# Kernel tuning notes

Measured on AMD Instinct MI355X. Metric: run time of the kernel, lower is better.

Reference implementation:

```python
import jax, jax.numpy as jnp
import numpy as np

B, S, HID = 1, 2048, 2048
H, HK, D, DV = 16, 4, 128, 128
ROPE = 64  # head_dim * partial_rotary_factor
SCALE = D ** -0.5


def _rotate_half(x):
    x1, x2 = x[..., : x.shape[-1] // 2], x[..., x.shape[-1] // 2:]
    return jnp.concatenate((-x2, x1), axis=-1)


def setup_inputs() -> dict:
    key = jax.random.key(0)
    ks = jax.random.split(key, 6)
    hidden_states = jax.random.normal(ks[0], (B, S, HID), dtype=jnp.float32)
    # real RoPE tables: positions x inv_freq over rope_dim, HF half-duplicated layout
    inv_freq = 1.0 / (10000.0 ** (jnp.arange(0, ROPE, 2, dtype=jnp.float32) / ROPE))
    ang = jnp.arange(S, dtype=jnp.float32)[:, None] * inv_freq[None, :]  # [S, ROPE/2]
    ang = jnp.concatenate([ang, ang], axis=-1)  # [S, ROPE]
    cos = jnp.broadcast_to(jnp.cos(ang)[None], (B, S, ROPE))
    sin = jnp.broadcast_to(jnp.sin(ang)[None], (B, S, ROPE))
    Wq = jax.random.normal(ks[1], (HID, H * D), dtype=jnp.float32) * 0.02
    Wk = jax.random.normal(ks[2], (HID, HK * D), dtype=jnp.float32) * 0.02
    Wv = jax.random.normal(ks[3], (HID, HK * DV), dtype=jnp.float32) * 0.02
    Wo = jax.random.normal(ks[4], (H * DV, HID), dtype=jnp.float32) * 0.02
    sink = jax.random.normal(ks[5], (H,), dtype=jnp.float32)
    return {"hidden_states": hidden_states, "cos": cos, "sin": sin,
            "Wq": Wq, "Wk": Wk, "Wv": Wv, "Wo": Wo, "sink": sink}


def reference(hidden_states, cos, sin, Wq, Wk, Wv, Wo, sink):
    b, s, _ = hidden_states.shape
    q = (hidden_states @ Wq).reshape(b, s, H, D).transpose(0, 2, 1, 3)    # [B,H,S,D]
    k = (hidden_states @ Wk).reshape(b, s, HK, D).transpose(0, 2, 1, 3)   # [B,HK,S,D]
    v = (hidden_states @ Wv).reshape(b, s, HK, DV).transpose(0, 2, 1, 3)  # [B,HK,S,DV]
    # partial RoPE on the first ROPE dims
    c = cos[:, None, :, :]  # [B,1,S,ROPE]
    sn = sin[:, None, :, :]
    q_r, q_n = q[..., :ROPE], q[..., ROPE:]
    k_r, k_n = k[..., :ROPE], k[..., ROPE:]
    q_r = q_r * c + _rotate_half(q_r) * sn
    k_r = k_r * c + _rotate_half(k_r) * sn
    q = jnp.concatenate([q_r, q_n], axis=-1)
    k = jnp.concatenate([k_r, k_n], axis=-1)
    # GQA: repeat kv heads
    g = H // HK
    k = jnp.broadcast_to(k[:, :, None], (b, HK, g, s, D)).reshape(b, H, s, D)
    v = jnp.broadcast_to(v[:, :, None], (b, HK, g, s, DV)).reshape(b, H, s, DV)
    scores = jnp.einsum("bhqd,bhkd->bhqk", q, k) * SCALE
    causal = jnp.triu(jnp.ones((s, s), dtype=bool), k=1)
    scores = jnp.where(causal[None, None], -jnp.inf, scores)
    # sink-bias softmax: sink logit joins the normalizer but gets no value
    m = jnp.max(scores, axis=-1, keepdims=True)                      # [B,H,S,1]
    sink_exp = jnp.exp(sink.reshape(1, H, 1, 1) - m)
    attn_exp = jnp.exp(scores - m)
    attn = attn_exp / (jnp.sum(attn_exp, axis=-1, keepdims=True) + sink_exp)
    out = jnp.einsum("bhqk,bhkv->bhqv", attn, v)                     # [B,H,S,DV]
    out = out.transpose(0, 2, 1, 3).reshape(b, s, H * DV)
    return out @ Wo
```

## Files before the change

### kernel.cpp

```cpp
#include <hip/hip_runtime.h>

#define S_LEN 2048
#define HID_D 2048
#define NH 16
#define NHK 4
#define HD 128
#define ATT_SCALE 0.08838834764831845f
#define NEG_INF (-3.0e38f)

typedef __attribute__((ext_vector_type(8))) __bf16 bf16x8;
typedef __attribute__((ext_vector_type(4))) __bf16 bf16x4;
typedef __attribute__((ext_vector_type(4))) float f32x4;

__device__ __forceinline__ void gload_lds16(const void* g, void* l) {
  __builtin_amdgcn_global_load_lds(
      (__attribute__((address_space(1))) void*)g,
      (__attribute__((address_space(3))) void*)l, 16, 0, 0);
}

__device__ __forceinline__ void transpose_job(
    const float* __restrict__ W, __bf16* __restrict__ WT, int K, int N,
    int local, int nbx, float* Ts ) {
  const int t = threadIdx.x;
  const int bk = (local / nbx) * 64, bn = (local % nbx) * 64;
  const int r = t >> 4, c4 = (t & 15) << 2;
#pragma unroll
  for (int i = 0; i < 4; ++i) {
    float4 v = *reinterpret_cast<const float4*>(
        &W[(size_t)(bk + r + 16 * i) * N + bn + c4]);
    *reinterpret_cast<float4*>(&Ts[(r + 16 * i) * 68 + c4]) = v;
  }
  __syncthreads();
#pragma unroll
  for (int i = 0; i < 4; ++i) {
    int n_l = r + 16 * i;
    bf16x4 o;
#pragma unroll
    for (int j = 0; j < 4; ++j) o[j] = (__bf16)Ts[(c4 + j) * 68 + n_l];
    *reinterpret_cast<bf16x4*>(&WT[(size_t)(bn + n_l) * K + bk + c4]) = o;
  }
}

__global__ __launch_bounds__(256) void prep_kernel(
    const float* __restrict__ hs, const float* __restrict__ Wq,
    const float* __restrict__ Wk, const float* __restrict__ Wv,
    const float* __restrict__ Wo, __bf16* __restrict__ hsb,
    __bf16* __restrict__ WqT, __bf16* __restrict__ WkT,
    __bf16* __restrict__ WvT, __bf16* __restrict__ WoT) {
  __shared__ float Ts[64 * 68];
  const int b = blockIdx.x;
  if (b < 4096) {
    int i = b * 256 + threadIdx.x;
    if (i < S_LEN * HID_D / 4) {
      float4 v = *reinterpret_cast<const float4*>(&hs[(size_t)i * 4]);
      bf16x4 o;
      o[0] = (__bf16)v.x; o[1] = (__bf16)v.y;
      o[2] = (__bf16)v.z; o[3] = (__bf16)v.w;
      *reinterpret_cast<bf16x4*>(&hsb[(size_t)i * 4]) = o;
    }
  } else if (b < 5120) {
    transpose_job(Wq, WqT, 2048, 2048, b - 4096, 32, Ts);
  } else if (b < 5376) {
    transpose_job(Wk, WkT, 2048, 512, b - 5120, 8, Ts);
  } else if (b < 5632) {
    transpose_job(Wv, WvT, 2048, 512, b - 5376, 8, Ts);
  } else {
    transpose_job(Wo, WoT, 2048, 2048, b - 5632, 32, Ts);
  }
}

template <int MODE>
__device__ __forceinline__ void mfma_gemm_tile_db(
    __bf16* As, __bf16* Bs,
    const __bf16* __restrict__ A, const __bf16* __restrict__ BT,
    float* __restrict__ C, __bf16* __restrict__ Db,
    const float* __restrict__ cs, const float* __restrict__ sn,
    int N, int K, int bm, int bn) {
  const int tid = threadIdx.x;
  const int wave = tid >> 6, lane = tid & 63;
  const int wr = (wave >> 1) * 64, wc = (wave & 1) * 64;
  const int l16 = lane & 15, lhi = lane >> 4;

  f32x4 acc[4][4];
#pragma unroll
  for (int i = 0; i < 4; ++i)
#pragma unroll
    for (int j = 0; j < 4; ++j) acc[i][j] = (f32x4){0.f, 0.f, 0.f, 0.f};

  const __bf16* Abase = A + (size_t)bm * K;
  const __bf16* Bbase = BT + (size_t)bn * K;
  const int nk = K >> 6;

  auto stage = [&](int buf, int k0) {
#pragma unroll
    for (int it = 0; it < 4; ++it) {
      int base = it * 256 + wave * 64;
      int f = base + lane;
      int row = f >> 3, ch = f & 7;
      gload_lds16(Abase + (size_t)row * K + k0 + ch * 8,
                  As + buf * 8192 + base * 8);
      gload_lds16(Bbase + (size_t)row * K + k0 + ch * 8,
                  Bs + buf * 8192 + base * 8);
    }
  };

  stage(0, 0);
  __syncthreads();
  for (int t = 0; t < nk; ++t) {
    const int buf = t & 1;
    if (t + 1 < nk) stage(buf ^ 1, (t + 1) * 64);
    const __bf16* Ab = As + buf * 8192;
    const __bf16* Bb = Bs + buf * 8192;
#pragma unroll
    for (int kk = 0; kk < 2; ++kk) {
      bf16x8 af[4], bfr[4];
#pragma unroll
      for (int i = 0; i < 4; ++i) {
        af[i] = *reinterpret_cast<const bf16x8*>(
            Ab + (wr + i * 16 + l16) * 64 + kk * 32 + lhi * 8);
        bfr[i] = *reinterpret_cast<const bf16x8*>(
            Bb + (wc + i * 16 + l16) * 64 + kk * 32 + lhi * 8);
      }
#pragma unroll
      for (int i = 0; i < 4; ++i)
#pragma unroll
        for (int j = 0; j < 4; ++j)
          acc[i][j] = __builtin_amdgcn_mfma_f32_16x16x32_bf16(
              af[i], bfr[j], acc[i][j], 0, 0, 0);
    }
    __syncthreads();
  }

  if (MODE == 0) {
#pragma unroll
    for (int i = 0; i < 4; ++i)
#pragma unroll
      for (int j = 0; j < 4; ++j)
#pragma unroll
        for (int r = 0; r < 4; ++r)
          C[(size_t)(bm + wr + i * 16 + lhi * 4 + r) * N + bn + wc + j * 16 +
            l16] = acc[i][j][r];
  } else if (MODE == 3) {
#pragma unroll
    for (int i = 0; i < 4; ++i)
#pragma unroll
      for (int j = 0; j < 4; ++j) {
        bf16x4 o;
#pragma unroll
        for (int r = 0; r < 4; ++r) o[r] = (__bf16)acc[i][j][r];
        *reinterpret_cast<bf16x4*>(
            &Db[(size_t)(bn + wc + j * 16 + l16) * S_LEN + bm + wr + i * 16 +
                lhi * 4]) = o;
      }
  } else {
    const int dst = (MODE == 1) ? (NH * HD) : (NHK * HD);
    if (wc == 0) {
#pragma unroll
      for (int i = 0; i < 4; ++i)
#pragma unroll
        for (int r = 0; r < 4; ++r) {
          int s = bm + wr + i * 16 + lhi * 4 + r;
          const float* cp = cs + (size_t)s * 64;
          const float* sp = sn + (size_t)s * 64;
          float c0 = cp[l16], c1 = cp[16 + l16];
          float c2 = cp[32 + l16], c3 = cp[48 + l16];
          float s0 = sp[l16], s1 = sp[16 + l16];
          float s2 = sp[32 + l16], s3 = sp[48 + l16];
          float x0 = acc[i][0][r], x1 = acc[i][1][r];
          float x2 = acc[i][2][r], x3 = acc[i][3][r];
          __bf16* dp = Db + (size_t)s * dst + bn;
          dp[l16]      = (__bf16)(x0 * c0 - x2 * s0);
          dp[16 + l16] = (__bf16)(x1 * c1 - x3 * s1);
          dp[32 + l16] = (__bf16)(x2 * c2 + x0 * s2);
          dp[48 + l16] = (__bf16)(x3 * c3 + x1 * s3);
        }
    } else {
#pragma unroll
      for (int i = 0; i < 4; ++i)
#pragma unroll
        for (int j = 0; j < 4; ++j)
#pragma unroll
          for (int r = 0; r < 4; ++r)
            Db[(size_t)(bm + wr + i * 16 + lhi * 4 + r) * dst + bn + wc +
               j * 16 + l16] = (__bf16)acc[i][j][r];
    }
  }
}

__global__ __launch_bounds__(256, 2) void qkv_gemm_kernel(
    const __bf16* __restrict__ hsb, const __bf16* __restrict__ WqT,
    const __bf16* __restrict__ WkT, const __bf16* __restrict__ WvT,
    __bf16* __restrict__ Qbf, __bf16* __restrict__ Kbf,
    __bf16* __restrict__ Vtb, const float* __restrict__ cs,
    const float* __restrict__ sn) {
  __shared__ __attribute__((aligned(16))) __bf16 As[2 * 8192];
  __shared__ __attribute__((aligned(16))) __bf16 Bs[2 * 8192];
  const int bx = blockIdx.x;
  const int bm = blockIdx.y * 128;
  if (bx < 16)
    mfma_gemm_tile_db<1>(As, Bs, hsb, WqT, nullptr, Qbf, cs, sn, 2048, HID_D,
                         bm, bx * 128);
  else if (bx < 20)
    mfma_gemm_tile_db<2>(As, Bs, hsb, WkT, nullptr, Kbf, cs, sn, 512, HID_D,
                         bm, (bx - 16) * 128);
  else
    mfma_gemm_tile_db<3>(As, Bs, hsb, WvT, nullptr, Vtb, cs, sn, 512, HID_D,
                         bm, (bx - 20) * 128);
}

__global__ __launch_bounds__(256, 2) void out_proj_kernel(
    const __bf16* __restrict__ Obf, const __bf16* __restrict__ WoT,
    float* __restrict__ out) {
  __shared__ __attribute__((aligned(16))) __bf16 As[2 * 8192];
  __shared__ __attribute__((aligned(16))) __bf16 Bs[2 * 8192];
  mfma_gemm_tile_db<0>(As, Bs, Obf, WoT, out, nullptr, nullptr, nullptr,
                       HID_D, NH * HD, blockIdx.y * 128, blockIdx.x * 128);
}

__device__ __forceinline__ unsigned pack2_bf16(float a, float b) {
  unsigned short lo = __builtin_bit_cast(unsigned short, (__bf16)a);
  unsigned short hi = __builtin_bit_cast(unsigned short, (__bf16)b);
  return (unsigned)lo | ((unsigned)hi << 16);
}

__global__ __launch_bounds__(256, 2) void attn_mfma_kernel(
    const __bf16* __restrict__ Qbf, const __bf16* __restrict__ Kbf,
    const __bf16* __restrict__ Vtb, const float* __restrict__ sink,
    __bf16* __restrict__ Obf) {
  __shared__ __attribute__((aligned(16))) __bf16 Ks[2 * 64 * 128];
  __shared__ __attribute__((aligned(16))) __bf16 Vs[2 * 128 * 64];

  const int tid = threadIdx.x;
  const int wave = tid >> 6, lane = tid & 63;
  const int l16 = lane & 15, lhi = lane >> 4;
  const int h = blockIdx.y;
  const int hk = h >> 2;
  const int qt = (h < 8) ? (31 - (int)blockIdx.x) : (int)blockIdx.x;
  const int q0 = qt * 64;
  const int qrow = q0 + wave * 16 + l16;

  bf16x8 qf[4];
  {
    const __bf16* qp = Qbf + (size_t)qrow * (NH * HD) + h * HD + lhi * 8;
#pragma unroll
    for (int d = 0; d < 4; ++d)
      qf[d] = *reinterpret_cast<const bf16x8*>(qp + d * 32);
  }

  float m = NEG_INF, l_ = 0.f;
  f32x4 acc[8];
#pragma unroll
  for (int f = 0; f < 8; ++f) acc[f] = (f32x4){0.f, 0.f, 0.f, 0.f};

  auto stage_kv = [&](int buf, int kt) {
#pragma unroll
    for (int it = 0; it < 4; ++it) {
      int base = it * 256 + wave * 64;
      int f = base + lane;
      {
        int row = f >> 4, ch = f & 15;
        int sch = (ch & 8) | ((ch ^ row) & 7);
        gload_lds16(Kbf + (size_t)(kt * 64 + row) * (NHK * HD) + hk * HD +
                        sch * 8,
                    Ks + buf * 8192 + base * 8);
      }
      {
        int dv = f >> 3, ch = f & 7;
        int sch = (ch ^ dv) & 7;
        gload_lds16(Vtb + (size_t)(hk * HD + dv) * S_LEN + kt * 64 + sch * 8,
                    Vs + buf * 8192 + base * 8);
      }
    }
  };

  const int xs7 = l16 & 7;
  const int nt = qt + 1;
  stage_kv(0, 0);
  __syncthreads();
  for (int kt = 0; kt < nt; ++kt) {
    const int buf = kt & 1;
    if (kt + 1 < nt) stage_kv(buf ^ 1, kt + 1);
    const __bf16* Kb_ = Ks + buf * 8192;
    const __bf16* Vb_ = Vs + buf * 8192;

    f32x4 sc[4];
#pragma unroll
    for (int kb = 0; kb < 4; ++kb) sc[kb] = (f32x4){0.f, 0.f, 0.f, 0.f};
#pragma unroll
    for (int d = 0; d < 4; ++d) {
#pragma unroll
      for (int kb = 0; kb < 4; ++kb) {
        int row = kb * 16 + l16;
        int ch = (d * 4 + lhi) ^ xs7;
        bf16x8 kf = *reinterpret_cast<const bf16x8*>(Kb_ + row * 128 + ch * 8);
        sc[kb] = __builtin_amdgcn_mfma_f32_16x16x32_bf16(kf, qf[d], sc[kb],
                                                         0, 0, 0);
      }
    }

    float s[4][4];
    const bool last = (kt == qt);
#pragma unroll
    for (int kb = 0; kb < 4; ++kb)
#pragma unroll
      for (int r = 0; r < 4; ++r) {
        float sv = sc[kb][r] * ATT_SCALE;
        if (last) {
          int kc = kt * 64 + kb * 16 + lhi * 4 + r;
          if (kc > qrow) sv = NEG_INF;
        }
        s[kb][r] = sv;
      }
    float tmax = s[0][0];
#pragma unroll
    for (int kb = 0; kb < 4; ++kb)
#pragma unroll
      for (int r = 0; r < 4; ++r) tmax = fmaxf(tmax, s[kb][r]);
    tmax = fmaxf(tmax, __shfl_xor(tmax, 16));
    tmax = fmaxf(tmax, __shfl_xor(tmax, 32));
    float mn = fmaxf(m, tmax);
    float fac = __expf(m - mn);
    m = mn;
    float p[4][4];
    float rs = 0.f;
#pragma unroll
    for (int kb = 0; kb < 4; ++kb)
#pragma unroll
      for (int r = 0; r < 4; ++r) {
        float pv = __expf(s[kb][r] - mn);
        p[kb][r] = pv;
        rs += pv;
      }
    rs += __shfl_xor(rs, 16);
    rs += __shfl_xor(rs, 32);
    l_ = l_ * fac + rs;

    float facb[4];
#pragma unroll
    for (int r = 0; r < 4; ++r) facb[r] = __shfl(fac, lhi * 4 + r);
#pragma unroll
    for (int f = 0; f < 8; ++f)
#pragma unroll
      for (int r = 0; r < 4; ++r) acc[f][r] *= facb[r];

    unsigned pk[4][2];
#pragma unroll
    for (int kb = 0; kb < 4; ++kb) {
      pk[kb][0] = pack2_bf16(p[kb][0], p[kb][1]);
      pk[kb][1] = pack2_bf16(p[kb][2], p[kb][3]);
    }
    const int s0 = l16 + 16 * (2 * (lhi & 1));
    const int s1 = s0 + 16;
    const bool hihalf = (lhi >= 2);
    bf16x8 pa[2];
#pragma unroll
    for (int c = 0; c < 2; ++c) {
      unsigned aw0 = __shfl((int)pk[2 * c][0], s0);
      unsigned aw1 = __shfl((int)pk[2 * c][1], s0);
      unsigned aw2 = __shfl((int)pk[2 * c][0], s1);
      unsigned aw3 = __shfl((int)pk[2 * c][1], s1);
      unsigned bw0 = __shfl((int)pk[2 * c + 1][0], s0);
      unsigned bw1 = __shfl((int)pk[2 * c + 1][1], s0);
      unsigned bw2 = __shfl((int)pk[2 * c + 1][0], s1);
      unsigned bw3 = __shfl((int)pk[2 * c + 1][1], s1);
      uint4 w;
      w.x = hihalf ? bw0 : aw0;
      w.y = hihalf ? bw1 : aw1;
      w.z = hihalf ? bw2 : aw2;
      w.w = hihalf ? bw3 : aw3;
      pa[c] = __builtin_bit_cast(bf16x8, w);
    }

#pragma unroll
    for (int c = 0; c < 2; ++c) {
#pragma unroll
      for (int dvf = 0; dvf < 8; ++dvf) {
        int row = dvf * 16 + l16;
        int ch = (c * 4 + lhi) ^ xs7;
        bf16x8 vf = *reinterpret_cast<const bf16x8*>(Vb_ + row * 64 + ch * 8);
        acc[dvf] = __builtin_amdgcn_mfma_f32_16x16x32_bf16(pa[c], vf, acc[dvf],
                                                           0, 0, 0);
      }
    }
    if (kt + 1 < nt) __syncthreads();
  }

  float inv = 1.0f / (l_ + __expf(sink[h] - m));
  float invb[4];
#pragma unroll
  for (int r = 0; r < 4; ++r) invb[r] = __shfl(inv, lhi * 4 + r);
#pragma unroll
  for (int dvf = 0; dvf < 8; ++dvf)
#pragma unroll
    for (int r = 0; r < 4; ++r) {
      int row = q0 + wave * 16 + lhi * 4 + r;
      Obf[(size_t)row * (NH * HD) + h * HD + dvf * 16 + l16] =
          (__bf16)(acc[dvf][r] * invb[r]);
    }
}

extern "C" void kernel_launch(void* const* d_in, const int* in_sizes, int n_in,
                              void* d_out, int out_size, void* d_ws,
                              size_t ws_size, hipStream_t stream) {
  const float* hs   = (const float*)d_in[0];
  const float* cosb = (const float*)d_in[1];
  const float* sinb = (const float*)d_in[2];
  const float* Wq   = (const float*)d_in[3];
  const float* Wk   = (const float*)d_in[4];
  const float* Wv   = (const float*)d_in[5];
  const float* Wo   = (const float*)d_in[6];
  const float* sink = (const float*)d_in[7];
  float* out = (float*)d_out;

  __bf16* hsb = (__bf16*)d_ws;
  __bf16* WqT = hsb + (size_t)S_LEN * HID_D;
  __bf16* WkT = WqT + (size_t)HID_D * (NH * HD);
  __bf16* WvT = WkT + (size_t)HID_D * (NHK * HD);
  __bf16* WoT = WvT + (size_t)HID_D * (NHK * HD);
  __bf16* Qbf = WoT + (size_t)(NH * HD) * HID_D;
  __bf16* Kbf = Qbf + (size_t)S_LEN * (NH * HD);
  __bf16* Vtb = Kbf + (size_t)S_LEN * (NHK * HD);
  __bf16* Obf = WqT;

  prep_kernel<<<dim3(6656), 256, 0, stream>>>(hs, Wq, Wk, Wv, Wo, hsb, WqT,
                                              WkT, WvT, WoT);
  qkv_gemm_kernel<<<dim3(24, 16), 256, 0, stream>>>(hsb, WqT, WkT, WvT, Qbf,
                                                    Kbf, Vtb, cosb, sinb);
  attn_mfma_kernel<<<dim3(32, 16), 256, 0, stream>>>(Qbf, Kbf, Vtb, sink, Obf);
  out_proj_kernel<<<dim3(16, 16), 256, 0, stream>>>(Obf, WoT, out);
}
```

Before: 274.8 us.

## Swizzle GEMM LDS layout, split-K out-projection, lazy softmax rescale

The GEMM LDS tiles are XOR-swizzled by row to cut bank conflicts on the fragment reads. The output projection becomes split-K over two z-slices that accumulate with float atomics into a buffer zeroed by a memset, which doubles the block count from 256 tiles. The attention online softmax now rescales the accumulator and running sum only when some row's max grows by more than 8, skipping the per-tile exp and rescale. The trade-offs are atomic traffic plus an extra memset, and a bounded risk of larger exponent values in the unnormalized accumulators.

```diff
diff --git a/kernel.cpp b/kernel.cpp
--- a/kernel.cpp
+++ b/kernel.cpp
@@ -75,11 +75,12 @@
     const __bf16* __restrict__ A, const __bf16* __restrict__ BT,
     float* __restrict__ C, __bf16* __restrict__ Db,
     const float* __restrict__ cs, const float* __restrict__ sn,
-    int N, int K, int bm, int bn) {
+    int N, int K, int bm, int bn, int kbeg, int ksteps) {
   const int tid = threadIdx.x;
   const int wave = tid >> 6, lane = tid & 63;
   const int wr = (wave >> 1) * 64, wc = (wave & 1) * 64;
   const int l16 = lane & 15, lhi = lane >> 4;
+  const int xs7 = l16 & 7;
 
   f32x4 acc[4][4];
 #pragma unroll
@@ -89,7 +90,6 @@
 
   const __bf16* Abase = A + (size_t)bm * K;
   const __bf16* Bbase = BT + (size_t)bn * K;
-  const int nk = K >> 6;
 
   auto stage = [&](int buf, int k0) {
 #pragma unroll
@@ -97,18 +97,19 @@
       int base = it * 256 + wave * 64;
       int f = base + lane;
       int row = f >> 3, ch = f & 7;
-      gload_lds16(Abase + (size_t)row * K + k0 + ch * 8,
+      int sch = (ch ^ row) & 7;
+      gload_lds16(Abase + (size_t)row * K + k0 + sch * 8,
                   As + buf * 8192 + base * 8);
-      gload_lds16(Bbase + (size_t)row * K + k0 + ch * 8,
+      gload_lds16(Bbase + (size_t)row * K + k0 + sch * 8,
                   Bs + buf * 8192 + base * 8);
     }
   };
 
-  stage(0, 0);
+  stage(0, kbeg);
   __syncthreads();
-  for (int t = 0; t < nk; ++t) {
+  for (int t = 0; t < ksteps; ++t) {
     const int buf = t & 1;
-    if (t + 1 < nk) stage(buf ^ 1, (t + 1) * 64);
+    if (t + 1 < ksteps) stage(buf ^ 1, kbeg + (t + 1) * 64);
     const __bf16* Ab = As + buf * 8192;
     const __bf16* Bb = Bs + buf * 8192;
 #pragma unroll
@@ -116,10 +117,11 @@
       bf16x8 af[4], bfr[4];
 #pragma unroll
       for (int i = 0; i < 4; ++i) {
+        int ch = (kk * 4 + lhi) ^ xs7;
         af[i] = *reinterpret_cast<const bf16x8*>(
-            Ab + (wr + i * 16 + l16) * 64 + kk * 32 + lhi * 8);
+            Ab + (wr + i * 16 + l16) * 64 + ch * 8);
         bfr[i] = *reinterpret_cast<const bf16x8*>(
-            Bb + (wc + i * 16 + l16) * 64 + kk * 32 + lhi * 8);
+            Bb + (wc + i * 16 + l16) * 64 + ch * 8);
       }
 #pragma unroll
       for (int i = 0; i < 4; ++i)
@@ -140,6 +142,16 @@
         for (int r = 0; r < 4; ++r)
           C[(size_t)(bm + wr + i * 16 + lhi * 4 + r) * N + bn + wc + j * 16 +
             l16] = acc[i][j][r];
+  } else if (MODE == 4) {
+#pragma unroll
+    for (int i = 0; i < 4; ++i)
+#pragma unroll
+      for (int j = 0; j < 4; ++j)
+#pragma unroll
+        for (int r = 0; r < 4; ++r)
+          atomicAdd(&C[(size_t)(bm + wr + i * 16 + lhi * 4 + r) * N + bn + wc +
+                       j * 16 + l16],
+                    acc[i][j][r]);
   } else if (MODE == 3) {
 #pragma unroll
     for (int i = 0; i < 4; ++i)
@@ -199,13 +211,13 @@
   const int bm = blockIdx.y * 128;
   if (bx < 16)
     mfma_gemm_tile_db<1>(As, Bs, hsb, WqT, nullptr, Qbf, cs, sn, 2048, HID_D,
-                         bm, bx * 128);
+                         bm, bx * 128, 0, 32);
   else if (bx < 20)
     mfma_gemm_tile_db<2>(As, Bs, hsb, WkT, nullptr, Kbf, cs, sn, 512, HID_D,
-                         bm, (bx - 16) * 128);
+                         bm, (bx - 16) * 128, 0, 32);
   else
     mfma_gemm_tile_db<3>(As, Bs, hsb, WvT, nullptr, Vtb, cs, sn, 512, HID_D,
-                         bm, (bx - 20) * 128);
+                         bm, (bx - 20) * 128, 0, 32);
 }
 
 __global__ __launch_bounds__(256, 2) void out_proj_kernel(
@@ -213,8 +225,9 @@
     float* __restrict__ out) {
   __shared__ __attribute__((aligned(16))) __bf16 As[2 * 8192];
   __shared__ __attribute__((aligned(16))) __bf16 Bs[2 * 8192];
-  mfma_gemm_tile_db<0>(As, Bs, Obf, WoT, out, nullptr, nullptr, nullptr,
-                       HID_D, NH * HD, blockIdx.y * 128, blockIdx.x * 128);
+  mfma_gemm_tile_db<4>(As, Bs, Obf, WoT, out, nullptr, nullptr, nullptr,
+                       HID_D, NH * HD, blockIdx.y * 128, blockIdx.x * 128,
+                       blockIdx.z * 1024, 16);
 }
 
 __device__ __forceinline__ unsigned pack2_bf16(float a, float b) {
@@ -318,30 +331,34 @@
       for (int r = 0; r < 4; ++r) tmax = fmaxf(tmax, s[kb][r]);
     tmax = fmaxf(tmax, __shfl_xor(tmax, 16));
     tmax = fmaxf(tmax, __shfl_xor(tmax, 32));
-    float mn = fmaxf(m, tmax);
-    float fac = __expf(m - mn);
-    m = mn;
+
+    if (!__all(tmax - m <= 8.0f)) {
+      float mn = fmaxf(m, tmax);
+      float fac = __expf(m - mn);
+      l_ *= fac;
+      float facb[4];
+#pragma unroll
+      for (int r = 0; r < 4; ++r) facb[r] = __shfl(fac, lhi * 4 + r);
+#pragma unroll
+      for (int f = 0; f < 8; ++f)
+#pragma unroll
+        for (int r = 0; r < 4; ++r) acc[f][r] *= facb[r];
+      m = mn;
+    }
+
     float p[4][4];
     float rs = 0.f;
 #pragma unroll
     for (int kb = 0; kb < 4; ++kb)
 #pragma unroll
       for (int r = 0; r < 4; ++r) {
-        float pv = __expf(s[kb][r] - mn);
+        float pv = __expf(s[kb][r] - m);
         p[kb][r] = pv;
         rs += pv;
       }
     rs += __shfl_xor(rs, 16);
     rs += __shfl_xor(rs, 32);
-    l_ = l_ * fac + rs;
-
-    float facb[4];
-#pragma unroll
-    for (int r = 0; r < 4; ++r) facb[r] = __shfl(fac, lhi * 4 + r);
-#pragma unroll
-    for (int f = 0; f < 8; ++f)
-#pragma unroll
-      for (int r = 0; r < 4; ++r) acc[f][r] *= facb[r];
+    l_ += rs;
 
     unsigned pk[4][2];
 #pragma unroll
@@ -427,5 +444,6 @@
   qkv_gemm_kernel<<<dim3(24, 16), 256, 0, stream>>>(hsb, WqT, WkT, WvT, Qbf,
                                                     Kbf, Vtb, cosb, sinb);
   attn_mfma_kernel<<<dim3(32, 16), 256, 0, stream>>>(Qbf, Kbf, Vtb, sink, Obf);
-  out_proj_kernel<<<dim3(16, 16), 256, 0, stream>>>(Obf, WoT, out);
-}
+  hipMemsetAsync(out, 0, (size_t)S_LEN * HID_D * sizeof(float), stream);
+  out_proj_kernel<<<dim3(16, 16, 2), 256, 0, stream>>>(Obf, WoT, out);
+}
```

Result: faster. 259.6 us (-5.5%).

## Shrink GEMM M-tile, swizzle LDS, single-buffer attention with lazy rescale and exp2

Applied to the files above, without the earlier changes.

The GEMM tiles drop from 128x128 to 64x128 so the grids double, and an XOR swizzle is added to the LDS layout to cut bank conflicts. The attention kernel moves from double-buffered to single-buffered K/V staging, which halves LDS use but exposes load latency on every tile. It also switches to exp2 with a prescaled log2e and skips the rescale of the accumulator unless the running max grows past a threshold. Priority hints are placed around the MFMA blocks. Together these are meant to raise occupancy and cut per-tile exponent and rescale work.

```diff
diff --git a/kernel.cpp b/kernel.cpp
--- a/kernel.cpp
+++ b/kernel.cpp
@@ -6,11 +6,15 @@
 #define NHK 4
 #define HD 128
 #define ATT_SCALE 0.08838834764831845f
+#define LOG2E 1.4426950408889634f
+#define SCALE2 (ATT_SCALE * LOG2E)
 #define NEG_INF (-3.0e38f)
 
 typedef __attribute__((ext_vector_type(8))) __bf16 bf16x8;
 typedef __attribute__((ext_vector_type(4))) __bf16 bf16x4;
 typedef __attribute__((ext_vector_type(4))) float f32x4;
+
+#define EXP2F(x) __builtin_amdgcn_exp2f(x)
 
 __device__ __forceinline__ void gload_lds16(const void* g, void* l) {
   __builtin_amdgcn_global_load_lds(
@@ -78,12 +82,13 @@
     int N, int K, int bm, int bn) {
   const int tid = threadIdx.x;
   const int wave = tid >> 6, lane = tid & 63;
-  const int wr = (wave >> 1) * 64, wc = (wave & 1) * 64;
+  const int wr = (wave >> 1) * 32, wc = (wave & 1) * 64;
   const int l16 = lane & 15, lhi = lane >> 4;
-
-  f32x4 acc[4][4];
-#pragma unroll
-  for (int i = 0; i < 4; ++i)
+  const int xs7 = l16 & 7;
+
+  f32x4 acc[2][4];
+#pragma unroll
+  for (int i = 0; i < 2; ++i)
 #pragma unroll
     for (int j = 0; j < 4; ++j) acc[i][j] = (f32x4){0.f, 0.f, 0.f, 0.f};
 
@@ -93,14 +98,21 @@
 
   auto stage = [&](int buf, int k0) {
 #pragma unroll
-    for (int it = 0; it < 4; ++it) {
+    for (int it = 0; it < 6; ++it) {
       int base = it * 256 + wave * 64;
       int f = base + lane;
-      int row = f >> 3, ch = f & 7;
-      gload_lds16(Abase + (size_t)row * K + k0 + ch * 8,
-                  As + buf * 8192 + base * 8);
-      gload_lds16(Bbase + (size_t)row * K + k0 + ch * 8,
-                  Bs + buf * 8192 + base * 8);
+      if (base < 512) {
+        int row = f >> 3, ch = f & 7;
+        int sch = (ch ^ row) & 7;
+        gload_lds16(Abase + (size_t)row * K + k0 + sch * 8,
+                    As + buf * 4096 + base * 8);
+      } else {
+        int g = f - 512;
+        int row = g >> 3, ch = g & 7;
+        int sch = (ch ^ row) & 7;
+        gload_lds16(Bbase + (size_t)row * K + k0 + sch * 8,
+                    Bs + buf * 8192 + (base - 512) * 8);
+      }
     }
   };
 
@@ -109,20 +121,22 @@
   for (int t = 0; t < nk; ++t) {
     const int buf = t & 1;
     if (t + 1 < nk) stage(buf ^ 1, (t + 1) * 64);
-    const __bf16* Ab = As + buf * 8192;
+    const __bf16* Ab = As + buf * 4096;
     const __bf16* Bb = Bs + buf * 8192;
 #pragma unroll
     for (int kk = 0; kk < 2; ++kk) {
-      bf16x8 af[4], bfr[4];
-#pragma unroll
-      for (int i = 0; i < 4; ++i) {
+      int ch = (kk * 4 + lhi) ^ xs7;
+      bf16x8 af[2], bfr[4];
+#pragma unroll
+      for (int i = 0; i < 2; ++i)
         af[i] = *reinterpret_cast<const bf16x8*>(
-            Ab + (wr + i * 16 + l16) * 64 + kk * 32 + lhi * 8);
-        bfr[i] = *reinterpret_cast<const bf16x8*>(
-            Bb + (wc + i * 16 + l16) * 64 + kk * 32 + lhi * 8);
-      }
-#pragma unroll
-      for (int i = 0; i < 4; ++i)
+            Ab + (wr + i * 16 + l16) * 64 + ch * 8);
+#pragma unroll
+      for (int j = 0; j < 4; ++j)
+        bfr[j] = *reinterpret_cast<const bf16x8*>(
+            Bb + (wc + j * 16 + l16) * 64 + ch * 8);
+#pragma unroll
+      for (int i = 0; i < 2; ++i)
 #pragma unroll
         for (int j = 0; j < 4; ++j)
           acc[i][j] = __builtin_amdgcn_mfma_f32_16x16x32_bf16(
@@ -133,7 +147,7 @@
 
   if (MODE == 0) {
 #pragma unroll
-    for (int i = 0; i < 4; ++i)
+    for (int i = 0; i < 2; ++i)
 #pragma unroll
       for (int j = 0; j < 4; ++j)
 #pragma unroll
@@ -142,7 +156,7 @@
             l16] = acc[i][j][r];
   } else if (MODE == 3) {
 #pragma unroll
-    for (int i = 0; i < 4; ++i)
+    for (int i = 0; i < 2; ++i)
 #pragma unroll
       for (int j = 0; j < 4; ++j) {
         bf16x4 o;
@@ -156,7 +170,7 @@
     const int dst = (MODE == 1) ? (NH * HD) : (NHK * HD);
     if (wc == 0) {
 #pragma unroll
-      for (int i = 0; i < 4; ++i)
+      for (int i = 0; i < 2; ++i)
 #pragma unroll
         for (int r = 0; r < 4; ++r) {
           int s = bm + wr + i * 16 + lhi * 4 + r;
@@ -176,7 +190,7 @@
         }
     } else {
 #pragma unroll
-      for (int i = 0; i < 4; ++i)
+      for (int i = 0; i < 2; ++i)
 #pragma unroll
         for (int j = 0; j < 4; ++j)
 #pragma unroll
@@ -193,10 +207,10 @@
     __bf16* __restrict__ Qbf, __bf16* __restrict__ Kbf,
     __bf16* __restrict__ Vtb, const float* __restrict__ cs,
     const float* __restrict__ sn) {
-  __shared__ __attribute__((aligned(16))) __bf16 As[2 * 8192];
+  __shared__ __attribute__((aligned(16))) __bf16 As[2 * 4096];
   __shared__ __attribute__((aligned(16))) __bf16 Bs[2 * 8192];
   const int bx = blockIdx.x;
-  const int bm = blockIdx.y * 128;
+  const int bm = blockIdx.y * 64;
   if (bx < 16)
     mfma_gemm_tile_db<1>(As, Bs, hsb, WqT, nullptr, Qbf, cs, sn, 2048, HID_D,
                          bm, bx * 128);
@@ -211,10 +225,10 @@
 __global__ __launch_bounds__(256, 2) void out_proj_kernel(
     const __bf16* __restrict__ Obf, const __bf16* __restrict__ WoT,
     float* __restrict__ out) {
-  __shared__ __attribute__((aligned(16))) __bf16 As[2 * 8192];
+  __shared__ __attribute__((aligned(16))) __bf16 As[2 * 4096];
   __shared__ __attribute__((aligned(16))) __bf16 Bs[2 * 8192];
   mfma_gemm_tile_db<0>(As, Bs, Obf, WoT, out, nullptr, nullptr, nullptr,
-                       HID_D, NH * HD, blockIdx.y * 128, blockIdx.x * 128);
+                       HID_D, NH * HD, blockIdx.y * 64, blockIdx.x * 128);
 }
 
 __device__ __forceinline__ unsigned pack2_bf16(float a, float b) {
@@ -227,8 +241,8 @@
     const __bf16* __restrict__ Qbf, const __bf16* __restrict__ Kbf,
     const __bf16* __restrict__ Vtb, const float* __restrict__ sink,
     __bf16* __restrict__ Obf) {
-  __shared__ __attribute__((aligned(16))) __bf16 Ks[2 * 64 * 128];
-  __shared__ __attribute__((aligned(16))) __bf16 Vs[2 * 128 * 64];
+  __shared__ __attribute__((aligned(16))) __bf16 Ks[64 * 128];
+  __shared__ __attribute__((aligned(16))) __bf16 Vs[128 * 64];
 
   const int tid = threadIdx.x;
   const int wave = tid >> 6, lane = tid & 63;
@@ -252,7 +266,9 @@
 #pragma unroll
   for (int f = 0; f < 8; ++f) acc[f] = (f32x4){0.f, 0.f, 0.f, 0.f};
 
-  auto stage_kv = [&](int buf, int kt) {
+  const int xs7 = l16 & 7;
+  const int nt = qt + 1;
+  for (int kt = 0; kt < nt; ++kt) {
 #pragma unroll
     for (int it = 0; it < 4; ++it) {
       int base = it * 256 + wave * 64;
@@ -262,41 +278,33 @@
         int sch = (ch & 8) | ((ch ^ row) & 7);
         gload_lds16(Kbf + (size_t)(kt * 64 + row) * (NHK * HD) + hk * HD +
                         sch * 8,
-                    Ks + buf * 8192 + base * 8);
+                    Ks + base * 8);
       }
       {
         int dv = f >> 3, ch = f & 7;
         int sch = (ch ^ dv) & 7;
         gload_lds16(Vtb + (size_t)(hk * HD + dv) * S_LEN + kt * 64 + sch * 8,
-                    Vs + buf * 8192 + base * 8);
-      }
-    }
-  };
-
-  const int xs7 = l16 & 7;
-  const int nt = qt + 1;
-  stage_kv(0, 0);
-  __syncthreads();
-  for (int kt = 0; kt < nt; ++kt) {
-    const int buf = kt & 1;
-    if (kt + 1 < nt) stage_kv(buf ^ 1, kt + 1);
-    const __bf16* Kb_ = Ks + buf * 8192;
-    const __bf16* Vb_ = Vs + buf * 8192;
+                    Vs + base * 8);
+      }
+    }
+    __syncthreads();
 
     f32x4 sc[4];
 #pragma unroll
     for (int kb = 0; kb < 4; ++kb) sc[kb] = (f32x4){0.f, 0.f, 0.f, 0.f};
+    __builtin_amdgcn_s_setprio(1);
 #pragma unroll
     for (int d = 0; d < 4; ++d) {
 #pragma unroll
       for (int kb = 0; kb < 4; ++kb) {
         int row = kb * 16 + l16;
         int ch = (d * 4 + lhi) ^ xs7;
-        bf16x8 kf = *reinterpret_cast<const bf16x8*>(Kb_ + row * 128 + ch * 8);
+        bf16x8 kf = *reinterpret_cast<const bf16x8*>(Ks + row * 128 + ch * 8);
         sc[kb] = __builtin_amdgcn_mfma_f32_16x16x32_bf16(kf, qf[d], sc[kb],
                                                          0, 0, 0);
       }
     }
+    __builtin_amdgcn_s_setprio(0);
 
     float s[4][4];
     const bool last = (kt == qt);
@@ -304,7 +312,7 @@
     for (int kb = 0; kb < 4; ++kb)
 #pragma unroll
       for (int r = 0; r < 4; ++r) {
-        float sv = sc[kb][r] * ATT_SCALE;
+        float sv = sc[kb][r] * SCALE2;
         if (last) {
           int kc = kt * 64 + kb * 16 + lhi * 4 + r;
           if (kc > qrow) sv = NEG_INF;
@@ -318,30 +326,34 @@
       for (int r = 0; r < 4; ++r) tmax = fmaxf(tmax, s[kb][r]);
     tmax = fmaxf(tmax, __shfl_xor(tmax, 16));
     tmax = fmaxf(tmax, __shfl_xor(tmax, 32));
-    float mn = fmaxf(m, tmax);
-    float fac = __expf(m - mn);
-    m = mn;
+
+    if (!__all(tmax - m <= 11.54f)) {
+      float mn = fmaxf(m, tmax);
+      float fac = EXP2F(m - mn);
+      l_ *= fac;
+      float facb[4];
+#pragma unroll
+      for (int r = 0; r < 4; ++r) facb[r] = __shfl(fac, lhi * 4 + r);
+#pragma unroll
+      for (int f = 0; f < 8; ++f)
+#pragma unroll
+        for (int r = 0; r < 4; ++r) acc[f][r] *= facb[r];
+      m = mn;
+    }
+
     float p[4][4];
     float rs = 0.f;
 #pragma unroll
     for (int kb = 0; kb < 4; ++kb)
 #pragma unroll
       for (int r = 0; r < 4; ++r) {
-        float pv = __expf(s[kb][r] - mn);
+        float pv = EXP2F(s[kb][r] - m);
         p[kb][r] = pv;
         rs += pv;
       }
     rs += __shfl_xor(rs, 16);
     rs += __shfl_xor(rs, 32);
-    l_ = l_ * fac + rs;
-
-    float facb[4];
-#pragma unroll
-    for (int r = 0; r < 4; ++r) facb[r] = __shfl(fac, lhi * 4 + r);
-#pragma unroll
-    for (int f = 0; f < 8; ++f)
-#pragma unroll
-      for (int r = 0; r < 4; ++r) acc[f][r] *= facb[r];
+    l_ += rs;
 
     unsigned pk[4][2];
 #pragma unroll
@@ -371,21 +383,23 @@
       pa[c] = __builtin_bit_cast(bf16x8, w);
     }
 
+    __builtin_amdgcn_s_setprio(1);
 #pragma unroll
     for (int c = 0; c < 2; ++c) {
 #pragma unroll
       for (int dvf = 0; dvf < 8; ++dvf) {
         int row = dvf * 16 + l16;
         int ch = (c * 4 + lhi) ^ xs7;
-        bf16x8 vf = *reinterpret_cast<const bf16x8*>(Vb_ + row * 64 + ch * 8);
+        bf16x8 vf = *reinterpret_cast<const bf16x8*>(Vs + row * 64 + ch * 8);
         acc[dvf] = __builtin_amdgcn_mfma_f32_16x16x32_bf16(pa[c], vf, acc[dvf],
                                                            0, 0, 0);
       }
     }
+    __builtin_amdgcn_s_setprio(0);
     if (kt + 1 < nt) __syncthreads();
   }
 
-  float inv = 1.0f / (l_ + __expf(sink[h] - m));
+  float inv = 1.0f / (l_ + EXP2F(sink[h] * LOG2E - m));
   float invb[4];
 #pragma unroll
   for (int r = 0; r < 4; ++r) invb[r] = __shfl(inv, lhi * 4 + r);
@@ -424,8 +438,8 @@
 
   prep_kernel<<<dim3(6656), 256, 0, stream>>>(hs, Wq, Wk, Wv, Wo, hsb, WqT,
                                               WkT, WvT, WoT);
-  qkv_gemm_kernel<<<dim3(24, 16), 256, 0, stream>>>(hsb, WqT, WkT, WvT, Qbf,
+  qkv_gemm_kernel<<<dim3(24, 32), 256, 0, stream>>>(hsb, WqT, WkT, WvT, Qbf,
                                                     Kbf, Vtb, cosb, sinb);
   attn_mfma_kernel<<<dim3(32, 16), 256, 0, stream>>>(Qbf, Kbf, Vtb, sink, Obf);
-  out_proj_kernel<<<dim3(16, 16), 256, 0, stream>>>(Obf, WoT, out);
-}
+  out_proj_kernel<<<dim3(16, 32), 256, 0, stream>>>(Obf, WoT, out);
+}
```

Measured after the change: 230.1 us. -16.2%, faster.
